# Optimization experiments

Hardware: AMD Instinct MI355X
Metric: run time of the kernel (lower is better)

## Reference

```python
import jax, jax.numpy as jnp
import numpy as np

N = 100000   # nodes
E = 1600000  # edges (avg degree 16)
R = 8        # relations
B = 4        # bases
IN = 128     # in_size
H = 128      # hidden_size
OUT = 64     # out_feats


def setup_inputs() -> dict:
    key = jax.random.key(0)
    k = jax.random.split(key, 14)
    sI = 1.0 / np.sqrt(IN)
    sH = 1.0 / np.sqrt(H)
    sB = 1.0 / np.sqrt(B)
    return {
        "feat": jax.random.normal(k[0], (N, IN), jnp.float32),
        "win": jax.random.normal(k[1], (IN, H), jnp.float32) * sI,
        "bin_": jnp.zeros((H,), jnp.float32),
        "basis0": jax.random.normal(k[2], (B, H, H), jnp.float32) * sH,
        "wcomp0": jax.random.normal(k[3], (R, B), jnp.float32) * sB,
        "loop0": jax.random.normal(k[4], (H, H), jnp.float32) * sH,
        "hbias0": jnp.zeros((H,), jnp.float32),
        "basis1": jax.random.normal(k[5], (B, H, H), jnp.float32) * sH,
        "wcomp1": jax.random.normal(k[6], (R, B), jnp.float32) * sB,
        "loop1": jax.random.normal(k[7], (H, H), jnp.float32) * sH,
        "hbias1": jnp.zeros((H,), jnp.float32),
        "wout": jax.random.normal(k[8], (H, OUT), jnp.float32) * sH,
        "bout": jnp.zeros((OUT,), jnp.float32),
        "src": jax.random.randint(k[9], (E,), 0, N),
        "dst": jax.random.randint(k[10], (E,), 0, N),
        "etypes": jax.random.randint(k[11], (E,), 0, R),
    }


def _rel_graph_conv(h, src, dst, etypes, basis, wcomp, loopw, hbias):
    """DGL RelGraphConv (basis regularizer, self_loop, bias, relu).

    out_i = relu( sum_r W_r * (sum_{e: dst_e=i, etype_e=r} h[src_e]) + h_i @ loopw + bias )
    Messages are linear, so we aggregate raw features by (dst, relation)
    composite key first, then apply the R per-relation matmuls once per node.
    """
    W = jnp.einsum('rb,bio->rio', wcomp, basis)          # [R, H, H] basis-composed weights
    seg = dst * R + etypes                               # composite (node, relation) key
    s = jax.ops.segment_sum(h[src], seg, num_segments=N * R)  # [N*R, H]
    s = s.reshape(N, R, -1)
    agg = jnp.einsum('nri,rio->no', s, W)                # [N, H]
    return jax.nn.relu(agg + hbias + h @ loopw)


def reference(feat, win, bin_, basis0, wcomp0, loop0, hbias0,
              basis1, wcomp1, loop1, hbias1, wout, bout, src, dst, etypes):
    h = jax.nn.relu(feat @ win + bin_)                   # input_layer
    h = _rel_graph_conv(h, src, dst, etypes, basis0, wcomp0, loop0, hbias0)
    h = _rel_graph_conv(h, src, dst, etypes, basis1, wcomp1, loop1, hbias1)
    return jax.nn.relu(h @ wout + bout)                  # out_layer
```

## Files before the change

### kernel.cpp

```cpp
#include <hip/hip_runtime.h>

#define NN   100000
#define EE   1600000
constexpr int RR = 8;
constexpr int BBASES = 4;
constexpr int SCAN_CHUNK = 1024;
constexpr int NBLK = (NN + SCAN_CHUNK - 1) / SCAN_CHUNK;
constexpr int NBUK = 98;
constexpr int EPB  = 4096;
constexpr int P1BLOCKS = (EE + EPB - 1) / EPB;

typedef __attribute__((ext_vector_type(8))) short short8;
typedef __attribute__((ext_vector_type(4))) float f32x4;

__device__ __forceinline__ unsigned pack2(float x, float y) {
    unsigned xu = __float_as_uint(x);
    unsigned yu = __float_as_uint(y);
    xu = (xu + 0x7fffu + ((xu >> 16) & 1u)) >> 16;
    yu = (yu + 0x7fffu + ((yu >> 16) & 1u)) & 0xffff0000u;
    return xu | yu;
}

__device__ __forceinline__ unsigned short bf16r(float x) {
    unsigned u = __float_as_uint(x);
    return (unsigned short)((u + 0x7fffu + ((u >> 16) & 1u)) >> 16);
}


__global__ __launch_bounds__(256) void count_kernel(const int* __restrict__ dst,
                                                    int* __restrict__ counts) {
    int e = blockIdx.x * 256 + threadIdx.x;
    if (e < EE) atomicAdd(&counts[dst[e]], 1);
}

__global__ __launch_bounds__(256) void scan1(const int* __restrict__ counts,
                                             int* __restrict__ offsets,
                                             int* __restrict__ totals) {
    __shared__ int lds[256];
    int b = blockIdx.x, tid = threadIdx.x;
    int base = b * SCAN_CHUNK + tid * 4;
    int v0 = (base + 0 < NN) ? counts[base + 0] : 0;
    int v1 = (base + 1 < NN) ? counts[base + 1] : 0;
    int v2 = (base + 2 < NN) ? counts[base + 2] : 0;
    int v3 = (base + 3 < NN) ? counts[base + 3] : 0;
    int s0 = v0, s1 = s0 + v1, s2 = s1 + v2, s3 = s2 + v3;
    lds[tid] = s3;
    __syncthreads();
    for (int d = 1; d < 256; d <<= 1) {
        int x = (tid >= d) ? lds[tid - d] : 0;
        __syncthreads();
        lds[tid] += x;
        __syncthreads();
    }
    int incl = lds[tid];
    int prefix = incl - s3;
    if (base + 0 < NN) offsets[base + 0] = prefix;
    if (base + 1 < NN) offsets[base + 1] = prefix + s0;
    if (base + 2 < NN) offsets[base + 2] = prefix + s1;
    if (base + 3 < NN) offsets[base + 3] = prefix + s2;
    if (tid == 255) totals[b] = lds[255];
}

__global__ void scan2(int* __restrict__ totals, int* __restrict__ offsets) {
    int run = 0;
    for (int b = 0; b < NBLK; ++b) { int x = totals[b]; totals[b] = run; run += x; }
    offsets[NN] = run;
}

__global__ __launch_bounds__(256) void scan3(int* __restrict__ offsets,
                                             const int* __restrict__ totals) {
    int i = blockIdx.x * 256 + threadIdx.x;
    if (i < NN) offsets[i] += totals[i >> 10];
}

__global__ void init_cursor(const int* __restrict__ offsets, int* __restrict__ gcursor) {
    int b = threadIdx.x;
    if (b < NBUK) gcursor[b] = offsets[b << 10];
}


__global__ __launch_bounds__(256) void bin_pass1(const int* __restrict__ src,
                                                 const int* __restrict__ dst,
                                                 const int* __restrict__ et,
                                                 int* __restrict__ gcursor,
                                                 unsigned* __restrict__ tmp) {
    __shared__ unsigned stage[EPB];
    __shared__ int hist[128];
    __shared__ int sc[128];
    __shared__ int lb[128];
    __shared__ int gb[128];
    int tid = threadIdx.x;
    long e0 = (long)blockIdx.x * EPB;
    if (tid < 128) hist[tid] = 0;
    __syncthreads();

    unsigned w[16];
    int bk[16], pos[16];
#pragma unroll
    for (int i = 0; i < 16; ++i) {
        long e = e0 + i * 256 + tid;
        bool valid = e < EE;
        int d = valid ? dst[e] : 0;
        int s = valid ? src[e] : 0;
        int r = valid ? et[e] : 0;
        bk[i] = d >> 10;
        w[i] = (unsigned)s | ((unsigned)r << 17) | ((unsigned)(d & 1023) << 20);
        pos[i] = valid ? atomicAdd(&hist[bk[i]], 1) : -1;
    }
    __syncthreads();
    if (tid < 128) sc[tid] = hist[tid];
    __syncthreads();
    for (int d = 1; d < 128; d <<= 1) {
        int v = 0;
        if (tid < 128 && tid >= d) v = sc[tid - d];
        __syncthreads();
        if (tid < 128) sc[tid] += v;
        __syncthreads();
    }
    if (tid < 128) lb[tid] = sc[tid] - hist[tid];
    if (tid < NBUK && hist[tid] > 0) gb[tid] = atomicAdd(&gcursor[tid], hist[tid]);
    __syncthreads();
    int total = sc[127];
#pragma unroll
    for (int i = 0; i < 16; ++i) {
        if (pos[i] >= 0) stage[lb[bk[i]] + pos[i]] = w[i];
    }
    __syncthreads();
    for (int s = tid; s < total; s += 256) {
        int lo = 0, hi = 127;
#pragma unroll
        for (int it = 0; it < 7; ++it) {
            int mid = (lo + hi + 1) >> 1;
            if (lb[mid] <= s) lo = mid; else hi = mid - 1;
        }
        tmp[gb[lo] + (s - lb[lo])] = stage[s];
    }
}

__global__ __launch_bounds__(1024) void bin_pass2(const unsigned* __restrict__ tmp,
                                                  const int* __restrict__ offsets,
                                                  int* __restrict__ packed) {
    __shared__ int cur[1024];
    __shared__ int offs[1025];
    int b = blockIdx.x, tid = threadIdx.x;
    int nb0 = b << 10;
    int nend = nb0 + 1024; if (nend > NN) nend = NN;
    int nloc = nend - nb0;
    cur[tid] = 0;
    for (int i = tid; i <= nloc; i += 1024) offs[i] = offsets[nb0 + i];
    __syncthreads();
    int beg = offs[0], end = offs[nloc];
    for (int e = beg + tid; e < end; e += 1024) {
        unsigned wv = tmp[e];
        int dl = (wv >> 20) & 1023;
        int p = offs[dl] + atomicAdd(&cur[dl], 1);
        packed[p] = (int)((wv & 0x1FFFFu) | (((wv >> 17) & 7u) << 20));
    }
}


__global__ __launch_bounds__(256) void convert_weights(const float* __restrict__ basis0,
                                                       const float* __restrict__ loop0,
                                                       const float* __restrict__ basis1,
                                                       const float* __restrict__ loop1,
                                                       const float* __restrict__ win,
                                                       const float* __restrict__ wout,
                                                       unsigned short* __restrict__ BT0,
                                                       unsigned short* __restrict__ BT1,
                                                       unsigned short* __restrict__ winT,
                                                       unsigned short* __restrict__ woutT) {
    int i = blockIdx.x * 256 + threadIdx.x;
    if (i < 81920) {
        int n = i / 640, k = i % 640;
        BT0[i] = bf16r(k < 512 ? basis0[(size_t)k * 128 + n] : loop0[(size_t)(k - 512) * 128 + n]);
    } else if (i < 163840) {
        int j = i - 81920;
        int n = j / 640, k = j % 640;
        BT1[j] = bf16r(k < 512 ? basis1[(size_t)k * 128 + n] : loop1[(size_t)(k - 512) * 128 + n]);
    } else if (i < 180224) {
        int j = i - 163840;
        int n = j >> 7, k = j & 127;
        winT[j] = bf16r(win[(size_t)k * 128 + n]);
    } else if (i < 188416) {
        int j = i - 180224;
        int n = j >> 7, k = j & 127;
        woutT[j] = bf16r(wout[(size_t)k * 64 + n]);
    }
}

template <int NC, bool F32OUT, bool AF32>
__global__ __launch_bounds__(256) void gemm128(const void* __restrict__ Aptr,
                                               const unsigned short* __restrict__ BT,
                                               const float* __restrict__ bias,
                                               void* __restrict__ outp, int M) {
    constexpr int NFRAG = NC / 32;
    constexpr int BQ = NC * 8 / 256;
    __shared__ char As[2][16384];
    __shared__ char Bs[2][NC * 128];
    int tid = threadIdx.x;
    int lane = tid & 63;
    int wave = tid >> 6;
    int wm = wave >> 1, wn = wave & 1;
    int m0 = blockIdx.x * 128;

    uint4 areg[4], breg[BQ];
    auto loadA = [&](int c) {
#pragma unroll
        for (int q = 0; q < 4; ++q) {
            int lin = q * 256 + tid;
            int row = lin >> 3, slot = lin & 7;
            int gr = m0 + row;
            gr = (gr < M) ? gr : (M - 1);
            if (AF32) {
                const float* fp = (const float*)Aptr + (size_t)gr * 128 + c * 64 + slot * 8;
                float4 v0 = *(const float4*)fp;
                float4 v1 = *(const float4*)(fp + 4);
                areg[q].x = pack2(v0.x, v0.y);
                areg[q].y = pack2(v0.z, v0.w);
                areg[q].z = pack2(v1.x, v1.y);
                areg[q].w = pack2(v1.z, v1.w);
            } else {
                areg[q] = *(const uint4*)((const char*)Aptr + (size_t)gr * 256 + c * 128 + slot * 16);
            }
        }
    };
    auto loadB = [&](int c) {
#pragma unroll
        for (int q = 0; q < BQ; ++q) {
            int lin = q * 256 + tid;
            int n = lin >> 3, slot = lin & 7;
            breg[q] = *(const uint4*)((const char*)BT + (size_t)n * 256 + c * 128 + slot * 16);
        }
    };

    f32x4 acc[4][NFRAG];
#pragma unroll
    for (int m = 0; m < 4; ++m)
#pragma unroll
        for (int n = 0; n < NFRAG; ++n) acc[m][n] = (f32x4)0.f;

    loadA(0); loadB(0);
    int swz = (lane & 7) << 4;

    for (int c = 0; c < 2; ++c) {
        int buf = c & 1;
#pragma unroll
        for (int q = 0; q < 4; ++q) {
            int lin = q * 256 + tid;
            int row = lin >> 3, slot = lin & 7;
            *(uint4*)(As[buf] + row * 128 + ((slot * 16) ^ ((row & 7) << 4))) = areg[q];
        }
#pragma unroll
        for (int q = 0; q < BQ; ++q) {
            int lin = q * 256 + tid;
            int row = lin >> 3, slot = lin & 7;
            *(uint4*)(Bs[buf] + row * 128 + ((slot * 16) ^ ((row & 7) << 4))) = breg[q];
        }
        __syncthreads();
        if (c < 1) { loadA(1); loadB(1); }
#pragma unroll
        for (int ks = 0; ks < 2; ++ks) {
            short8 a[4], b[NFRAG];
            int kb = ks * 64 + (lane >> 4) * 16;
#pragma unroll
            for (int m = 0; m < 4; ++m) {
                int row = wm * 64 + m * 16 + (lane & 15);
                a[m] = *(const short8*)(As[buf] + row * 128 + (kb ^ swz));
            }
#pragma unroll
            for (int n = 0; n < NFRAG; ++n) {
                int col = wn * (NC / 2) + n * 16 + (lane & 15);
                b[n] = *(const short8*)(Bs[buf] + col * 128 + (kb ^ swz));
            }
#pragma unroll
            for (int m = 0; m < 4; ++m)
#pragma unroll
                for (int n = 0; n < NFRAG; ++n)
                    acc[m][n] = __builtin_amdgcn_mfma_f32_16x16x32_bf16(a[m], b[n], acc[m][n], 0, 0, 0);
        }
        __syncthreads();
    }

    int colbase = wn * (NC / 2) + (lane & 15);
    float bias_v[NFRAG];
#pragma unroll
    for (int n = 0; n < NFRAG; ++n) bias_v[n] = bias[colbase + n * 16];
#pragma unroll
    for (int m = 0; m < 4; ++m) {
        int rl0 = m0 + wm * 64 + m * 16 + ((lane >> 4) << 2);
#pragma unroll
        for (int n = 0; n < NFRAG; ++n) {
            int col = colbase + n * 16;
#pragma unroll
            for (int q = 0; q < 4; ++q) {
                float v = fmaxf(acc[m][n][q] + bias_v[n], 0.f);
                int row = rl0 + q;
                if (F32OUT) {
                    if (row < M) ((float*)outp)[(size_t)row * NC + col] = v;
                } else {
                    float vo = __shfl_xor(v, 1);
                    if (((lane & 1) == 0) && row < M)
                        ((unsigned*)outp)[(size_t)row * (NC / 2) + (col >> 1)] = pack2(v, vo);
                }
            }
        }
    }
}


__global__ __launch_bounds__(256) void agg_kernel(const unsigned* __restrict__ hin,
                                                  const int* __restrict__ offsets,
                                                  const int* __restrict__ packed,
                                                  const float* __restrict__ wcomp,
                                                  unsigned* __restrict__ tbuf,
                                                  int chunk_start, int chunk_len) {
    __shared__ float wc[32];
    int tid = threadIdx.x;
    if (tid < 32) wc[tid] = wcomp[tid];
    __syncthreads();
    int nl = blockIdx.x * 4 + (tid >> 6);
    int lane = tid & 63;
    if (nl >= chunk_len) return;
    int n = chunk_start + nl;
    int beg = offsets[n], end = offsets[n + 1];
    float a0x = 0.f, a0y = 0.f, a1x = 0.f, a1y = 0.f;
    float a2x = 0.f, a2y = 0.f, a3x = 0.f, a3y = 0.f;
    auto edge = [&](unsigned u, unsigned hv) {
        int r = (int)(u >> 20);
        float hx = __uint_as_float(hv << 16);
        float hy = __uint_as_float(hv & 0xffff0000u);
        float w0 = wc[r * 4 + 0], w1 = wc[r * 4 + 1];
        float w2 = wc[r * 4 + 2], w3 = wc[r * 4 + 3];
        a0x = fmaf(w0, hx, a0x); a0y = fmaf(w0, hy, a0y);
        a1x = fmaf(w1, hx, a1x); a1y = fmaf(w1, hy, a1y);
        a2x = fmaf(w2, hx, a2x); a2y = fmaf(w2, hy, a2y);
        a3x = fmaf(w3, hx, a3x); a3y = fmaf(w3, hy, a3y);
    };
    int e = beg;
    for (; e + 4 <= end; e += 4) {
        unsigned u0 = (unsigned)packed[e + 0];
        unsigned u1 = (unsigned)packed[e + 1];
        unsigned u2 = (unsigned)packed[e + 2];
        unsigned u3 = (unsigned)packed[e + 3];
        unsigned h0 = hin[(size_t)(u0 & 0xFFFFFu) * 64 + lane];
        unsigned h1 = hin[(size_t)(u1 & 0xFFFFFu) * 64 + lane];
        unsigned h2 = hin[(size_t)(u2 & 0xFFFFFu) * 64 + lane];
        unsigned h3 = hin[(size_t)(u3 & 0xFFFFFu) * 64 + lane];
        edge(u0, h0); edge(u1, h1); edge(u2, h2); edge(u3, h3);
    }
    for (; e < end; ++e) {
        unsigned u = (unsigned)packed[e];
        unsigned hv = hin[(size_t)(u & 0xFFFFFu) * 64 + lane];
        edge(u, hv);
    }
    size_t tb = (size_t)nl * 256 + lane;
    tbuf[tb + 0]   = pack2(a0x, a0y);
    tbuf[tb + 64]  = pack2(a1x, a1y);
    tbuf[tb + 128] = pack2(a2x, a2y);
    tbuf[tb + 192] = pack2(a3x, a3y);
}


__global__ __launch_bounds__(256) void conv_gemm(const unsigned* __restrict__ tbuf,
                                                 const unsigned* __restrict__ hin,
                                                 const unsigned short* __restrict__ BT,
                                                 const float* __restrict__ hbias,
                                                 unsigned* __restrict__ hout,
                                                 int chunk_start, int chunk_len) {
    __shared__ char As[2][16384];
    __shared__ char Bs[2][16384];
    int tid = threadIdx.x;
    int lane = tid & 63;
    int wave = tid >> 6;
    int wm = wave >> 1, wn = wave & 1;
    int m0 = blockIdx.x * 128;

    uint4 areg[4], breg[4];

    auto loadA = [&](int c) {
#pragma unroll
        for (int q = 0; q < 4; ++q) {
            int lin = q * 256 + tid;
            int row = lin >> 3, slot = lin & 7;
            int lr = m0 + row;
            lr = (lr < chunk_len) ? lr : (chunk_len - 1);
            const char* srcp;
            if (c < 8)
                srcp = (const char*)(tbuf + (size_t)lr * 256) + c * 128 + slot * 16;
            else
                srcp = (const char*)(hin + (size_t)(chunk_start + lr) * 64) + (c - 8) * 128 + slot * 16;
            areg[q] = *(const uint4*)srcp;
        }
    };
    auto loadB = [&](int c) {
#pragma unroll
        for (int q = 0; q < 4; ++q) {
            int lin = q * 256 + tid;
            int n = lin >> 3, slot = lin & 7;
            breg[q] = *(const uint4*)((const char*)(BT + (size_t)n * 640) + c * 128 + slot * 16);
        }
    };

    f32x4 acc[4][4];
#pragma unroll
    for (int m = 0; m < 4; ++m)
#pragma unroll
        for (int n = 0; n < 4; ++n) acc[m][n] = (f32x4)0.f;

    loadA(0); loadB(0);
    int swz = (lane & 7) << 4;

    for (int c = 0; c < 10; ++c) {
        int buf = c & 1;
#pragma unroll
        for (int q = 0; q < 4; ++q) {
            int lin = q * 256 + tid;
            int row = lin >> 3, slot = lin & 7;
            int off = row * 128 + ((slot * 16) ^ ((row & 7) << 4));
            *(uint4*)(As[buf] + off) = areg[q];
            *(uint4*)(Bs[buf] + off) = breg[q];
        }
        __syncthreads();
        if (c < 9) { loadA(c + 1); loadB(c + 1); }
#pragma unroll
        for (int ks = 0; ks < 2; ++ks) {
            short8 a[4], b[4];
            int kb = ks * 64 + (lane >> 4) * 16;
#pragma unroll
            for (int m = 0; m < 4; ++m) {
                int row = wm * 64 + m * 16 + (lane & 15);
                a[m] = *(const short8*)(As[buf] + row * 128 + (kb ^ swz));
            }
#pragma unroll
            for (int n = 0; n < 4; ++n) {
                int col = wn * 64 + n * 16 + (lane & 15);
                b[n] = *(const short8*)(Bs[buf] + col * 128 + (kb ^ swz));
            }
#pragma unroll
            for (int m = 0; m < 4; ++m)
#pragma unroll
                for (int n = 0; n < 4; ++n)
                    acc[m][n] = __builtin_amdgcn_mfma_f32_16x16x32_bf16(a[m], b[n], acc[m][n], 0, 0, 0);
        }
        __syncthreads();
    }

    int colbase = wn * 64 + (lane & 15);
    float bias_v[4];
#pragma unroll
    for (int n = 0; n < 4; ++n) bias_v[n] = hbias[colbase + n * 16];
#pragma unroll
    for (int m = 0; m < 4; ++m) {
        int rl0 = m0 + wm * 64 + m * 16 + ((lane >> 4) << 2);
#pragma unroll
        for (int n = 0; n < 4; ++n) {
            int col = colbase + n * 16;
#pragma unroll
            for (int q = 0; q < 4; ++q) {
                float v = fmaxf(acc[m][n][q] + bias_v[n], 0.f);
                float vo = __shfl_xor(v, 1);
                int lr = rl0 + q;
                if (((lane & 1) == 0) && lr < chunk_len) {
                    hout[(size_t)(chunk_start + lr) * 64 + (col >> 1)] = pack2(v, vo);
                }
            }
        }
    }
}


static inline size_t align256(size_t x) { return (x + 255) & ~(size_t)255; }

extern "C" void kernel_launch(void* const* d_in, const int* in_sizes, int n_in,
                              void* d_out, int out_size, void* d_ws, size_t ws_size,
                              hipStream_t stream) {
    const float* feat   = (const float*)d_in[0];
    const float* win    = (const float*)d_in[1];
    const float* bin_   = (const float*)d_in[2];
    const float* basis0 = (const float*)d_in[3];
    const float* wcomp0 = (const float*)d_in[4];
    const float* loop0  = (const float*)d_in[5];
    const float* hbias0 = (const float*)d_in[6];
    const float* basis1 = (const float*)d_in[7];
    const float* wcomp1 = (const float*)d_in[8];
    const float* loop1  = (const float*)d_in[9];
    const float* hbias1 = (const float*)d_in[10];
    const float* wout   = (const float*)d_in[11];
    const float* bout   = (const float*)d_in[12];
    const int*   src    = (const int*)d_in[13];
    const int*   dst    = (const int*)d_in[14];
    const int*   etyp   = (const int*)d_in[15];
    float* outp = (float*)d_out;

    size_t off = 0;
    char* wsb = (char*)d_ws;
    auto walloc = [&](size_t bytes) { void* p = wsb + off; off += align256(bytes); return p; };
    unsigned* hA  = (unsigned*)walloc((size_t)NN * 64 * 4);
    unsigned* hB  = (unsigned*)walloc((size_t)NN * 64 * 4);
    int* offsets  = (int*)walloc((size_t)(NN + 1) * 4);
    int* counts   = (int*)walloc((size_t)NN * 4);
    int* totals   = (int*)walloc((size_t)NBLK * 4);
    int* gcursor  = (int*)walloc((size_t)NBUK * 4);
    int* packed   = (int*)walloc((size_t)EE * 4);
    unsigned* tmp = (unsigned*)walloc((size_t)EE * 4);
    unsigned short* BT0 = (unsigned short*)walloc((size_t)128 * 640 * 2);
    unsigned short* BT1 = (unsigned short*)walloc((size_t)128 * 640 * 2);
    unsigned short* winT = (unsigned short*)walloc((size_t)128 * 128 * 2);
    unsigned short* woutT = (unsigned short*)walloc((size_t)64 * 128 * 2);
    size_t fixed = off;

    int nchunk = 1;
    while (nchunk < 32) {
        size_t rows = (size_t)(NN + nchunk - 1) / nchunk;
        if (fixed + rows * 1024 <= ws_size) break;
        nchunk *= 2;
    }
    int chunk_rows = (NN + nchunk - 1) / nchunk;
    unsigned* tbuf = (unsigned*)(wsb + fixed);

    hipMemsetAsync(counts, 0, (size_t)NN * 4, stream);
    count_kernel<<<(EE + 255) / 256, 256, 0, stream>>>(dst, counts);
    scan1<<<NBLK, 256, 0, stream>>>(counts, offsets, totals);
    scan2<<<1, 1, 0, stream>>>(totals, offsets);
    scan3<<<(NN + 255) / 256, 256, 0, stream>>>(offsets, totals);
    init_cursor<<<1, 128, 0, stream>>>(offsets, gcursor);
    bin_pass1<<<P1BLOCKS, 256, 0, stream>>>(src, dst, etyp, gcursor, tmp);
    bin_pass2<<<NBUK, 1024, 0, stream>>>(tmp, offsets, packed);

    convert_weights<<<(188416 + 255) / 256, 256, 0, stream>>>(
        basis0, loop0, basis1, loop1, win, wout, BT0, BT1, winT, woutT);

    int gblocks = (NN + 127) / 128;
    gemm128<128, false, true><<<gblocks, 256, 0, stream>>>(feat, winT, bin_, hA, NN);

    for (int s = 0; s < NN; s += chunk_rows) {
        int len = (NN - s < chunk_rows) ? (NN - s) : chunk_rows;
        agg_kernel<<<(len + 3) / 4, 256, 0, stream>>>(hA, offsets, packed, wcomp0, tbuf, s, len);
        conv_gemm<<<(len + 127) / 128, 256, 0, stream>>>(tbuf, hA, BT0, hbias0, hB, s, len);
    }
    for (int s = 0; s < NN; s += chunk_rows) {
        int len = (NN - s < chunk_rows) ? (NN - s) : chunk_rows;
        agg_kernel<<<(len + 3) / 4, 256, 0, stream>>>(hB, offsets, packed, wcomp1, tbuf, s, len);
        conv_gemm<<<(len + 127) / 128, 256, 0, stream>>>(tbuf, hB, BT1, hbias1, hA, s, len);
    }
    gemm128<64, true, false><<<gblocks, 256, 0, stream>>>(hA, woutT, bout, outp, NN);
}
```

Measured before the change: 491.6 us.

## Use async global-to-LDS loads in conv_gemm, per-relation sums in aggregation

The aggregation kernel now accumulates raw per-relation sums through a wave-uniform switch and applies the basis coefficients once per node at the end, cutting per-edge FMAs from eight to two. The conv_gemm staging replaces register-staged loads and LDS stores with global_load_lds async copies that pre-swizzle the source addresses. Its epilogue stages output through LDS so global stores become coalesced 16-byte writes. Risks include the readfirstlane assumption on relation type (true, since all lanes handle the same edge) and the correctness of the swizzle and sync ordering for the async copies.

```diff
diff --git a/kernel.cpp b/kernel.cpp
--- a/kernel.cpp
+++ b/kernel.cpp
@@ -24,6 +24,12 @@
 __device__ __forceinline__ unsigned short bf16r(float x) {
     unsigned u = __float_as_uint(x);
     return (unsigned short)((u + 0x7fffu + ((u >> 16) & 1u)) >> 16);
+}
+
+__device__ __forceinline__ void async16(const void* g, void* l) {
+    __builtin_amdgcn_global_load_lds(
+        (const __attribute__((address_space(1))) void*)g,
+        (__attribute__((address_space(3))) void*)l, 16, 0, 0);
 }
 
 
@@ -195,8 +201,8 @@
                                                void* __restrict__ outp, int M) {
     constexpr int NFRAG = NC / 32;
     constexpr int BQ = NC * 8 / 256;
-    __shared__ char As[2][16384];
-    __shared__ char Bs[2][NC * 128];
+    __shared__ __align__(16) char As[2][16384];
+    __shared__ __align__(16) char Bs[2][NC * 128];
     int tid = threadIdx.x;
     int lane = tid & 63;
     int wave = tid >> 6;
@@ -323,18 +329,24 @@
     if (nl >= chunk_len) return;
     int n = chunk_start + nl;
     int beg = offsets[n], end = offsets[n + 1];
-    float a0x = 0.f, a0y = 0.f, a1x = 0.f, a1y = 0.f;
-    float a2x = 0.f, a2y = 0.f, a3x = 0.f, a3y = 0.f;
-    auto edge = [&](unsigned u, unsigned hv) {
-        int r = (int)(u >> 20);
+    float s0x = 0.f, s0y = 0.f, s1x = 0.f, s1y = 0.f;
+    float s2x = 0.f, s2y = 0.f, s3x = 0.f, s3y = 0.f;
+    float s4x = 0.f, s4y = 0.f, s5x = 0.f, s5y = 0.f;
+    float s6x = 0.f, s6y = 0.f, s7x = 0.f, s7y = 0.f;
+    auto acc_edge = [&](unsigned u, unsigned hv) {
+        int r = __builtin_amdgcn_readfirstlane((int)(u >> 20));
         float hx = __uint_as_float(hv << 16);
         float hy = __uint_as_float(hv & 0xffff0000u);
-        float w0 = wc[r * 4 + 0], w1 = wc[r * 4 + 1];
-        float w2 = wc[r * 4 + 2], w3 = wc[r * 4 + 3];
-        a0x = fmaf(w0, hx, a0x); a0y = fmaf(w0, hy, a0y);
-        a1x = fmaf(w1, hx, a1x); a1y = fmaf(w1, hy, a1y);
-        a2x = fmaf(w2, hx, a2x); a2y = fmaf(w2, hy, a2y);
-        a3x = fmaf(w3, hx, a3x); a3y = fmaf(w3, hy, a3y);
+        switch (r) {
+            case 0: s0x += hx; s0y += hy; break;
+            case 1: s1x += hx; s1y += hy; break;
+            case 2: s2x += hx; s2y += hy; break;
+            case 3: s3x += hx; s3y += hy; break;
+            case 4: s4x += hx; s4y += hy; break;
+            case 5: s5x += hx; s5y += hy; break;
+            case 6: s6x += hx; s6y += hy; break;
+            default: s7x += hx; s7y += hy; break;
+        }
     };
     int e = beg;
     for (; e + 4 <= end; e += 4) {
@@ -346,18 +358,27 @@
         unsigned h1 = hin[(size_t)(u1 & 0xFFFFFu) * 64 + lane];
         unsigned h2 = hin[(size_t)(u2 & 0xFFFFFu) * 64 + lane];
         unsigned h3 = hin[(size_t)(u3 & 0xFFFFFu) * 64 + lane];
-        edge(u0, h0); edge(u1, h1); edge(u2, h2); edge(u3, h3);
+        acc_edge(u0, h0); acc_edge(u1, h1); acc_edge(u2, h2); acc_edge(u3, h3);
     }
     for (; e < end; ++e) {
         unsigned u = (unsigned)packed[e];
         unsigned hv = hin[(size_t)(u & 0xFFFFFu) * 64 + lane];
-        edge(u, hv);
-    }
+        acc_edge(u, hv);
+    }
+    float sx[8] = {s0x, s1x, s2x, s3x, s4x, s5x, s6x, s7x};
+    float sy[8] = {s0y, s1y, s2y, s3y, s4y, s5y, s6y, s7y};
     size_t tb = (size_t)nl * 256 + lane;
-    tbuf[tb + 0]   = pack2(a0x, a0y);
-    tbuf[tb + 64]  = pack2(a1x, a1y);
-    tbuf[tb + 128] = pack2(a2x, a2y);
-    tbuf[tb + 192] = pack2(a3x, a3y);
+#pragma unroll
+    for (int b = 0; b < BBASES; ++b) {
+        float ax = 0.f, ay = 0.f;
+#pragma unroll
+        for (int r = 0; r < RR; ++r) {
+            float w = wc[r * 4 + b];
+            ax = fmaf(w, sx[r], ax);
+            ay = fmaf(w, sy[r], ay);
+        }
+        tbuf[tb + b * 64] = pack2(ax, ay);
+    }
 }
 
 
@@ -367,39 +388,29 @@
                                                  const float* __restrict__ hbias,
                                                  unsigned* __restrict__ hout,
                                                  int chunk_start, int chunk_len) {
-    __shared__ char As[2][16384];
-    __shared__ char Bs[2][16384];
+    __shared__ __align__(16) char As[2][16384];
+    __shared__ __align__(16) char Bs[2][16384];
     int tid = threadIdx.x;
     int lane = tid & 63;
     int wave = tid >> 6;
     int wm = wave >> 1, wn = wave & 1;
     int m0 = blockIdx.x * 128;
 
-    uint4 areg[4], breg[4];
-
-    auto loadA = [&](int c) {
+    auto stage = [&](int c, int buf) {
 #pragma unroll
         for (int q = 0; q < 4; ++q) {
-            int lin = q * 256 + tid;
-            int row = lin >> 3, slot = lin & 7;
+            int row = q * 32 + wave * 8 + (lane >> 3);
+            int s_src = (lane & 7) ^ (lane >> 3);
             int lr = m0 + row;
             lr = (lr < chunk_len) ? lr : (chunk_len - 1);
-            const char* srcp;
-            if (c < 8)
-                srcp = (const char*)(tbuf + (size_t)lr * 256) + c * 128 + slot * 16;
-            else
-                srcp = (const char*)(hin + (size_t)(chunk_start + lr) * 64) + (c - 8) * 128 + slot * 16;
-            areg[q] = *(const uint4*)srcp;
+            const char* ga = (c < 8)
+                ? (const char*)(tbuf + (size_t)lr * 256) + c * 128 + s_src * 16
+                : (const char*)(hin + (size_t)(chunk_start + lr) * 64) + (c - 8) * 128 + s_src * 16;
+            async16(ga, &As[buf][q * 4096 + wave * 1024]);
+            const char* gb = (const char*)BT + (size_t)row * 1280 + c * 128 + s_src * 16;
+            async16(gb, &Bs[buf][q * 4096 + wave * 1024]);
         }
     };
-    auto loadB = [&](int c) {
-#pragma unroll
-        for (int q = 0; q < 4; ++q) {
-            int lin = q * 256 + tid;
-            int n = lin >> 3, slot = lin & 7;
-            breg[q] = *(const uint4*)((const char*)(BT + (size_t)n * 640) + c * 128 + slot * 16);
-        }
-    };
 
     f32x4 acc[4][4];
 #pragma unroll
@@ -407,21 +418,13 @@
 #pragma unroll
         for (int n = 0; n < 4; ++n) acc[m][n] = (f32x4)0.f;
 
-    loadA(0); loadB(0);
+    stage(0, 0);
+    __syncthreads();
     int swz = (lane & 7) << 4;
 
     for (int c = 0; c < 10; ++c) {
         int buf = c & 1;
-#pragma unroll
-        for (int q = 0; q < 4; ++q) {
-            int lin = q * 256 + tid;
-            int row = lin >> 3, slot = lin & 7;
-            int off = row * 128 + ((slot * 16) ^ ((row & 7) << 4));
-            *(uint4*)(As[buf] + off) = areg[q];
-            *(uint4*)(Bs[buf] + off) = breg[q];
-        }
-        __syncthreads();
-        if (c < 9) { loadA(c + 1); loadB(c + 1); }
+        if (c < 9) stage(c + 1, buf ^ 1);
 #pragma unroll
         for (int ks = 0; ks < 2; ++ks) {
             short8 a[4], b[4];
@@ -445,25 +448,34 @@
         __syncthreads();
     }
 
+    unsigned* olds = (unsigned*)&As[0][0];
     int colbase = wn * 64 + (lane & 15);
     float bias_v[4];
 #pragma unroll
     for (int n = 0; n < 4; ++n) bias_v[n] = hbias[colbase + n * 16];
 #pragma unroll
     for (int m = 0; m < 4; ++m) {
-        int rl0 = m0 + wm * 64 + m * 16 + ((lane >> 4) << 2);
+        int rbase = wm * 64 + m * 16 + ((lane >> 4) << 2);
 #pragma unroll
         for (int n = 0; n < 4; ++n) {
-            int col = colbase + n * 16;
 #pragma unroll
             for (int q = 0; q < 4; ++q) {
                 float v = fmaxf(acc[m][n][q] + bias_v[n], 0.f);
                 float vo = __shfl_xor(v, 1);
-                int lr = rl0 + q;
-                if (((lane & 1) == 0) && lr < chunk_len) {
-                    hout[(size_t)(chunk_start + lr) * 64 + (col >> 1)] = pack2(v, vo);
+                if ((lane & 1) == 0) {
+                    olds[(rbase + q) * 64 + wn * 32 + n * 8 + ((lane & 15) >> 1)] = pack2(v, vo);
                 }
             }
+        }
+    }
+    __syncthreads();
+#pragma unroll
+    for (int i = 0; i < 8; ++i) {
+        int j = i * 256 + tid;
+        int row = j >> 4, s = j & 15;
+        int gr = m0 + row;
+        if (gr < chunk_len) {
+            ((uint4*)(hout + (size_t)(chunk_start + gr) * 64))[s] = ((const uint4*)olds)[j];
         }
     }
 }
```

Result: slower. 1.207 ms (+145.5%).
